# Kernel optimization log

Measured on AMD Instinct MI355X. Metric: run time of the kernel, lower is better.

Reference implementation:

```python
import jax, jax.numpy as jnp
import numpy as np
import math

N_HEADS = 16
EPS = 1e-6


def rmsnorm(x, w):
    xf = x.astype(jnp.float32)
    n = xf * jax.lax.rsqrt(jnp.mean(xf * xf, axis=-1, keepdims=True) + EPS)
    return n.astype(x.dtype) * w


def setup_inputs() -> dict:
    key = jax.random.key(0)
    ks = jax.random.split(key, 8)
    B, T, C, Hf = 1, 4096, 1024, 4096
    s = lambda fan_in: 1.0 / math.sqrt(fan_in)
    return {
        "x": jax.random.normal(ks[0], (B, T, C), jnp.float32),
        "attn_norm_w": jnp.ones((C,), jnp.float32),
        "ffn_norm_w": jnp.ones((C,), jnp.float32),
        "c_attn_w": jax.random.normal(ks[1], (3 * C, C), jnp.float32) * s(C),
        "c_proj_w": jax.random.normal(ks[2], (C, C), jnp.float32) * s(C),
        "w1": jax.random.normal(ks[3], (Hf, C), jnp.float32) * s(C),
        "w2": jax.random.normal(ks[4], (C, Hf), jnp.float32) * s(Hf),
        "w3": jax.random.normal(ks[5], (Hf, C), jnp.float32) * s(C),
    }


def attention(x, c_attn_w, c_proj_w):
    B, T, C = x.shape
    hd = C // N_HEADS
    qkv = x @ c_attn_w.T  # [B,T,3C]
    q, k, v = jnp.split(qkv, 3, axis=-1)
    q = q.reshape(B, T, N_HEADS, hd).transpose(0, 2, 1, 3)  # [B,H,T,hd]
    k = k.reshape(B, T, N_HEADS, hd).transpose(0, 2, 1, 3)
    v = v.reshape(B, T, N_HEADS, hd).transpose(0, 2, 1, 3)
    att = jnp.einsum('bhqd,bhkd->bhqk', q, k) * (1.0 / math.sqrt(hd))
    mask = jnp.tril(jnp.ones((T, T), bool))  # causal
    att = jnp.where(mask, att, -jnp.inf)
    att = jax.nn.softmax(att, axis=-1)
    y = jnp.einsum('bhqk,bhkd->bhqd', att, v)
    y = y.transpose(0, 2, 1, 3).reshape(B, T, C)
    return y @ c_proj_w.T


def ffn(x, w1, w2, w3):
    return (jax.nn.silu(x @ w1.T) * (x @ w3.T)) @ w2.T


def reference(x, attn_norm_w, ffn_norm_w, c_attn_w, c_proj_w, w1, w2, w3):
    x = x + attention(rmsnorm(x, attn_norm_w), c_attn_w, c_proj_w)
    x = x + ffn(rmsnorm(x, ffn_norm_w), w1, w2, w3)
    return x
```

## Files before the change

### kernel.cpp

```cpp
#include <hip/hip_runtime.h>
#include <hip/hip_bf16.h>

typedef __hip_bfloat16 bf16;
typedef __bf16 bf16r;
typedef bf16r bf16x8 __attribute__((ext_vector_type(8)));
typedef bf16r bf16x4 __attribute__((ext_vector_type(4)));
typedef float f32x4 __attribute__((ext_vector_type(4)));

#define T_SEQ 4096
#define C_DIM 1024
#define LD_QKV 3072
#define MB(x) ((size_t)(x) << 20)
#define SCL 0.18033688011112042f

#define AS1 __attribute__((address_space(1)))
#define AS3 __attribute__((address_space(3)))

static __device__ __forceinline__ unsigned short f2bf(float f) {
    bf16 h = (bf16)f;
    return *reinterpret_cast<unsigned short*>(&h);
}

__global__ __launch_bounds__(256) void cvt_w(const float* __restrict__ src, size_t eoff,
                                             ushort4* __restrict__ dst, int n4,
                                             int n4scl, float scl) {
    int i = blockIdx.x * 256 + threadIdx.x;
    const int stride = gridDim.x * 256;
    const float4* s = (const float4*)(src + eoff);
    for (; i < n4; i += stride) {
        float4 v = s[i];
        const float m = (i < n4scl) ? scl : 1.0f;
        ushort4 o;
        o.x = f2bf(v.x * m); o.y = f2bf(v.y * m); o.z = f2bf(v.z * m); o.w = f2bf(v.w * m);
        dst[i] = o;
    }
}

__global__ __launch_bounds__(256) void cvt_w13(const float* __restrict__ s1,
                                               const float* __restrict__ s3,
                                               ushort4* __restrict__ d1,
                                               ushort4* __restrict__ d3, int n4) {
    int i = blockIdx.x * 256 + threadIdx.x;
    const int stride = gridDim.x * 256;
    for (; i < n4; i += stride) {
        float4 v1 = ((const float4*)s1)[i];
        float4 v3 = ((const float4*)s3)[i];
        ushort4 o1, o3;
        o1.x = f2bf(v1.x); o1.y = f2bf(v1.y); o1.z = f2bf(v1.z); o1.w = f2bf(v1.w);
        o3.x = f2bf(v3.x); o3.y = f2bf(v3.y); o3.z = f2bf(v3.z); o3.w = f2bf(v3.w);
        d1[i] = o1;
        d3[i] = o3;
    }
}

__global__ __launch_bounds__(256) void copy_f32(const float4* __restrict__ src,
                                                float4* __restrict__ dst, int n4) {
    int i = blockIdx.x * 256 + threadIdx.x;
    const int stride = gridDim.x * 256;
    for (; i < n4; i += stride) dst[i] = src[i];
}

__global__ __launch_bounds__(256) void rmsnorm_k(const float* __restrict__ x,
                                                 const float* __restrict__ w,
                                                 bf16* __restrict__ out) {
    const int row = blockIdx.x;
    const int tid = threadIdx.x;
    const float* xr = x + (size_t)row * C_DIM;
    float v[4];
    float ss = 0.f;
#pragma unroll
    for (int i = 0; i < 4; i++) { v[i] = xr[tid * 4 + i]; ss += v[i] * v[i]; }
#pragma unroll
    for (int off = 32; off; off >>= 1) ss += __shfl_xor(ss, off);
    __shared__ float red[4];
    if ((tid & 63) == 0) red[tid >> 6] = ss;
    __syncthreads();
    const float tot = red[0] + red[1] + red[2] + red[3];
    const float scale = rsqrtf(tot * (1.0f / C_DIM) + 1e-6f);
#pragma unroll
    for (int i = 0; i < 4; i++) {
        const int c = tid * 4 + i;
        out[(size_t)row * C_DIM + c] = (bf16)(v[i] * scale * w[c]);
    }
}

template <int RESID, int OUTF32>
__global__ __launch_bounds__(256) void gemm128(const bf16* __restrict__ A, int lda,
                                               const bf16* __restrict__ B, int ldb,
                                               const void* __restrict__ resid,
                                               void* __restrict__ out,
                                               int N, int K) {
    __shared__ __align__(16) bf16r As[128 * 64];
    __shared__ __align__(16) bf16r Bs[128 * 64];
    const int tid = threadIdx.x;
    const int w = tid >> 6, lane = tid & 63;
    const int c = lane & 15, qd = lane >> 4;
    const int wm = w >> 1, wn = w & 1;
    const int mbase = blockIdx.y * 128;
    const int nbase = blockIdx.x * 128;
    const size_t koff = (size_t)blockIdx.z * K;

    const int srow = lane >> 3, schk = lane & 7;
    const bf16* gA = A + (size_t)(mbase + srow) * lda + schk * 8 + koff;
    const bf16* gB = B + (size_t)(nbase + srow) * ldb + schk * 8 + koff;

    f32x4 acc[4][4] = {};

    for (int k0 = 0; k0 < K; k0 += 64) {
        __syncthreads();
#pragma unroll
        for (int g = 0; g < 4; g++) {
            const int grp = w * 4 + g;
            __builtin_amdgcn_global_load_lds(
                (const AS1 void*)(gA + (size_t)(grp * 8) * lda + k0),
                (AS3 void*)&As[grp * 8 * 64], 16, 0, 0);
            __builtin_amdgcn_global_load_lds(
                (const AS1 void*)(gB + (size_t)(grp * 8) * ldb + k0),
                (AS3 void*)&Bs[grp * 8 * 64], 16, 0, 0);
        }
        __syncthreads();

#pragma unroll
        for (int kk = 0; kk < 2; kk++) {
            bf16x8 a[4], b[4];
#pragma unroll
            for (int i = 0; i < 4; i++)
                a[i] = *(const bf16x8*)&As[(wm * 64 + i * 16 + c) * 64 + kk * 32 + qd * 8];
#pragma unroll
            for (int j = 0; j < 4; j++)
                b[j] = *(const bf16x8*)&Bs[(wn * 64 + j * 16 + c) * 64 + kk * 32 + qd * 8];
#pragma unroll
            for (int i = 0; i < 4; i++)
#pragma unroll
                for (int j = 0; j < 4; j++)
                    acc[i][j] = __builtin_amdgcn_mfma_f32_16x16x32_bf16(a[i], b[j], acc[i][j], 0, 0, 0);
        }
    }

#pragma unroll
    for (int i = 0; i < 4; i++) {
#pragma unroll
        for (int j = 0; j < 4; j++) {
            const int col = nbase + wn * 64 + j * 16 + c;
#pragma unroll
            for (int reg = 0; reg < 4; reg++) {
                const int row = mbase + wm * 64 + i * 16 + qd * 4 + reg;
                const size_t idx = (size_t)row * N + col;
                float v = acc[i][j][reg];
                if (RESID == 2) v += ((const float*)resid)[idx];
                if (RESID == 3) {
                    const float a1 = (float)((const bf16*)resid)[idx];
                    v = (a1 / (1.0f + __expf(-a1))) * v;
                }
                if (RESID == 4) {
                    atomicAdd(&((float*)out)[idx], v);
                } else if (OUTF32) {
                    ((float*)out)[idx] = v;
                } else {
                    ((bf16*)out)[idx] = (bf16)v;
                }
            }
        }
    }
}

__global__ __launch_bounds__(256, 2) void gemm_w13(const bf16* __restrict__ A,
                                                   const bf16* __restrict__ B1,
                                                   const bf16* __restrict__ B3,
                                                   bf16* __restrict__ out,
                                                   int N, int K) {
    __shared__ __align__(16) bf16r As[128 * 64];
    __shared__ __align__(16) bf16r B1s[128 * 64];
    __shared__ __align__(16) bf16r B3s[128 * 64];
    const int tid = threadIdx.x;
    const int w = tid >> 6, lane = tid & 63;
    const int c = lane & 15, qd = lane >> 4;
    const int wm = w >> 1, wn = w & 1;
    const int mbase = blockIdx.y * 128;
    const int nbase = blockIdx.x * 128;

    const int srow = lane >> 3, schk = lane & 7;
    const bf16* gA = A + (size_t)(mbase + srow) * K + schk * 8;
    const bf16* gB1 = B1 + (size_t)(nbase + srow) * K + schk * 8;
    const bf16* gB3 = B3 + (size_t)(nbase + srow) * K + schk * 8;

    f32x4 acc1[4][4] = {};
    f32x4 acc3[4][4] = {};

    for (int k0 = 0; k0 < K; k0 += 64) {
        __syncthreads();
#pragma unroll
        for (int g = 0; g < 4; g++) {
            const int grp = w * 4 + g;
            __builtin_amdgcn_global_load_lds(
                (const AS1 void*)(gA + (size_t)(grp * 8) * K + k0),
                (AS3 void*)&As[grp * 8 * 64], 16, 0, 0);
            __builtin_amdgcn_global_load_lds(
                (const AS1 void*)(gB1 + (size_t)(grp * 8) * K + k0),
                (AS3 void*)&B1s[grp * 8 * 64], 16, 0, 0);
            __builtin_amdgcn_global_load_lds(
                (const AS1 void*)(gB3 + (size_t)(grp * 8) * K + k0),
                (AS3 void*)&B3s[grp * 8 * 64], 16, 0, 0);
        }
        __syncthreads();

#pragma unroll
        for (int kk = 0; kk < 2; kk++) {
            bf16x8 a[4], b1[4], b3[4];
#pragma unroll
            for (int i = 0; i < 4; i++)
                a[i] = *(const bf16x8*)&As[(wm * 64 + i * 16 + c) * 64 + kk * 32 + qd * 8];
#pragma unroll
            for (int j = 0; j < 4; j++) {
                b1[j] = *(const bf16x8*)&B1s[(wn * 64 + j * 16 + c) * 64 + kk * 32 + qd * 8];
                b3[j] = *(const bf16x8*)&B3s[(wn * 64 + j * 16 + c) * 64 + kk * 32 + qd * 8];
            }
#pragma unroll
            for (int i = 0; i < 4; i++)
#pragma unroll
                for (int j = 0; j < 4; j++) {
                    acc1[i][j] = __builtin_amdgcn_mfma_f32_16x16x32_bf16(a[i], b1[j], acc1[i][j], 0, 0, 0);
                    acc3[i][j] = __builtin_amdgcn_mfma_f32_16x16x32_bf16(a[i], b3[j], acc3[i][j], 0, 0, 0);
                }
        }
    }

#pragma unroll
    for (int i = 0; i < 4; i++) {
#pragma unroll
        for (int j = 0; j < 4; j++) {
            const int col = nbase + wn * 64 + j * 16 + c;
#pragma unroll
            for (int reg = 0; reg < 4; reg++) {
                const int row = mbase + wm * 64 + i * 16 + qd * 4 + reg;
                const float a1 = acc1[i][j][reg];
                const float h = (a1 / (1.0f + __expf(-a1))) * acc3[i][j][reg];
                out[(size_t)row * N + col] = (bf16)h;
            }
        }
    }
}

#define CTR_STRIDE 16
__global__ __launch_bounds__(256) void build_tr(const bf16* __restrict__ qkv,
                                                bf16* __restrict__ dst, int soff,
                                                int* __restrict__ ctrs) {
    if (blockIdx.x == 0 && blockIdx.y == 0 && threadIdx.x < 8 * CTR_STRIDE)
        ctrs[threadIdx.x] = 0;
    const int h = blockIdx.y;
    const int tb = blockIdx.x;
    __shared__ bf16 tile[64][65];
    const int tx = threadIdx.x & 63;
    const int ty = threadIdx.x >> 6;
    for (int rr = ty; rr < 64; rr += 4)
        tile[rr][tx] = qkv[(size_t)(tb * 64 + rr) * LD_QKV + soff + h * 64 + tx];
    __syncthreads();
    for (int rr = ty; rr < 64; rr += 4)
        dst[((size_t)h * 64 + rr) * T_SEQ + tb * 64 + tx] = tile[tx][rr];
}

__global__ __launch_bounds__(256) void attn_mfma(const bf16* __restrict__ qkv,
                                                 const bf16* __restrict__ VT,
                                                 bf16* __restrict__ y,
                                                 int* __restrict__ ctrs) {
    __shared__ __align__(16) bf16r Ks[128][64];
    __shared__ __align__(16) bf16r VTs[64][128];
    __shared__ __align__(16) bf16r Ps[4][16][128];
    __shared__ int s_wi;

    const int tid  = threadIdx.x;
    const int w    = tid >> 6;
    const int lane = tid & 63;
    const int c    = lane & 15;
    const int qd   = lane >> 4;
    const int sw   = c & 7;
    const int qi   = blockIdx.x & 7;
    int* ctr = ctrs + qi * CTR_STRIDE;

    while (true) {
        __syncthreads();
        if (tid == 0) s_wi = atomicAdd(ctr, 1);
        __syncthreads();
        const int j = s_wi;
        if (j >= 128) break;

        const int h    = qi + 8 * (j & 1);
        const int qb   = 63 - (j >> 1);
        const int qrow = qb * 64 + w * 16 + c;

        bf16x8 qf[2];
        {
            const bf16* qp = qkv + (size_t)qrow * LD_QKV + h * 64;
            qf[0] = *(const bf16x8*)(qp + qd * 8);
            qf[1] = *(const bf16x8*)(qp + 32 + qd * 8);
        }

        f32x4 O[4] = {};
        float m_i = -1e30f, l_i = 0.f;
        const int nkb = (qb >> 1) + 1;

        for (int kb = 0; kb < nkb; kb++) {
            __syncthreads();
#pragma unroll
            for (int ii = 0; ii < 4; ii++) {
                const int i = ii * 256 + tid;
                const int kr = i >> 3, ch = i & 7;
                *(bf16x8*)&Ks[kr][(ch ^ (kr & 7)) * 8] =
                    *(const bf16x8*)(qkv + (size_t)(kb * 128 + kr) * LD_QKV + C_DIM + h * 64 + ch * 8);
                const int vr = i >> 4, vch = i & 15;
                *(bf16x8*)&VTs[vr][(vch ^ (vr & 7)) * 8] =
                    *(const bf16x8*)(VT + ((size_t)h * 64 + vr) * T_SEQ + kb * 128 + vch * 8);
            }
            __syncthreads();

            f32x4 ST[8];
#pragma unroll
            for (int kt = 0; kt < 8; kt++) {
                f32x4 z = {};
#pragma unroll
                for (int ks = 0; ks < 2; ks++) {
                    bf16x8 kf = *(const bf16x8*)&Ks[kt * 16 + c][((ks * 4 + qd) ^ sw) * 8];
                    z = __builtin_amdgcn_mfma_f32_16x16x32_bf16(kf, qf[ks], z, 0, 0, 0);
                }
                ST[kt] = z;
            }

            if (kb == nkb - 1) {
#pragma unroll
                for (int kt = 0; kt < 8; kt++)
#pragma unroll
                    for (int r = 0; r < 4; r++)
                        if (kb * 128 + kt * 16 + qd * 4 + r > qrow) ST[kt][r] = -1e30f;
            }

            float mb = -1e30f;
#pragma unroll
            for (int kt = 0; kt < 8; kt++)
#pragma unroll
                for (int r = 0; r < 4; r++) mb = fmaxf(mb, ST[kt][r]);
            mb = fmaxf(mb, __shfl_xor(mb, 16));
            mb = fmaxf(mb, __shfl_xor(mb, 32));

            bf16x4 pv[8];
            float rs = 0.f;
            if (__all(mb - m_i <= 8.0f)) {
#pragma unroll
                for (int kt = 0; kt < 8; kt++)
#pragma unroll
                    for (int r = 0; r < 4; r++) {
                        const float p = exp2f(ST[kt][r] - m_i);
                        pv[kt][r] = (bf16r)p;
                        rs += p;
                    }
                rs += __shfl_xor(rs, 16);
                rs += __shfl_xor(rs, 32);
                l_i += rs;
            } else {
                const float mnew = fmaxf(m_i, mb);
                const float alpha = exp2f(m_i - mnew);
#pragma unroll
                for (int kt = 0; kt < 8; kt++)
#pragma unroll
                    for (int r = 0; r < 4; r++) {
                        const float p = exp2f(ST[kt][r] - mnew);
                        pv[kt][r] = (bf16r)p;
                        rs += p;
                    }
                rs += __shfl_xor(rs, 16);
                rs += __shfl_xor(rs, 32);
                l_i = l_i * alpha + rs;
                m_i = mnew;
#pragma unroll
                for (int dt = 0; dt < 4; dt++)
#pragma unroll
                    for (int r = 0; r < 4; r++) O[dt][r] *= alpha;
            }

#pragma unroll
            for (int kt = 0; kt < 8; kt++) {
                const int phys = (kt * 2 + (qd >> 1)) ^ sw;
                *(bf16x4*)&Ps[w][c][phys * 8 + (qd & 1) * 4] = pv[kt];
            }

#pragma unroll
            for (int ks = 0; ks < 4; ks++) {
                bf16x8 pf = *(const bf16x8*)&Ps[w][c][((ks * 4 + qd) ^ sw) * 8];
#pragma unroll
                for (int dt = 0; dt < 4; dt++) {
                    bf16x8 vf = *(const bf16x8*)&VTs[dt * 16 + c][((ks * 4 + qd) ^ sw) * 8];
                    O[dt] = __builtin_amdgcn_mfma_f32_16x16x32_bf16(vf, pf, O[dt], 0, 0, 0);
                }
            }
        }

        const float inv_l = 1.0f / l_i;
#pragma unroll
        for (int dt = 0; dt < 4; dt++) {
            bf16x4 ov;
#pragma unroll
            for (int r = 0; r < 4; r++) ov[r] = (bf16r)(O[dt][r] * inv_l);
            *(bf16x4*)(y + (size_t)qrow * C_DIM + h * 64 + dt * 16 + qd * 4) = ov;
        }
    }
}

extern "C" void kernel_launch(void* const* d_in, const int* in_sizes, int n_in,
                              void* d_out, int out_size, void* d_ws, size_t ws_size,
                              hipStream_t stream) {
    const float* x        = (const float*)d_in[0];
    const float* attn_w   = (const float*)d_in[1];
    const float* ffn_w    = (const float*)d_in[2];
    const float* c_attn_w = (const float*)d_in[3];
    const float* c_proj_w = (const float*)d_in[4];
    const float* w1       = (const float*)d_in[5];
    const float* w2       = (const float*)d_in[6];
    const float* w3       = (const float*)d_in[7];
    float* xmid = (float*)d_out;

    char* ws = (char*)d_ws;
    bf16* cwA  = (bf16*)(ws);
    bf16* cwP  = (bf16*)(ws + MB(6));
    bf16* rms1 = (bf16*)(ws + MB(8));
    bf16* qkv  = (bf16*)(ws + MB(16));
    bf16* VT   = (bf16*)(ws + MB(40));
    bf16* y    = (bf16*)(ws + MB(48));
    int*  ctrs = (int*)(ws + MB(8));
    bf16* rms2 = (bf16*)(ws);
    bf16* w1h  = (bf16*)(ws + MB(8));
    bf16* w3h  = (bf16*)(ws + MB(16));
    bf16* w2h  = (bf16*)(ws + MB(8));
    bf16* h1   = (bf16*)(ws + MB(24));

    cvt_w<<<512, 256, 0, stream>>>(c_attn_w, 0, (ushort4*)cwA, 3072 * 1024 / 4,
                                   1024 * 1024 / 4, SCL);
    cvt_w<<<512, 256, 0, stream>>>(c_proj_w, 0, (ushort4*)cwP, 1024 * 1024 / 4, 0, 1.0f);
    rmsnorm_k<<<T_SEQ, 256, 0, stream>>>(x, attn_w, rms1);
    gemm128<0, 0><<<dim3(24, 32), 256, 0, stream>>>(rms1, C_DIM, cwA, C_DIM, nullptr, qkv, 3072, 1024);
    build_tr<<<dim3(64, 16), 256, 0, stream>>>(qkv, VT, 2 * C_DIM, ctrs);
    attn_mfma<<<768, 256, 0, stream>>>(qkv, VT, y, ctrs);
    cvt_w13<<<512, 256, 0, stream>>>(w1, w3, (ushort4*)w1h, (ushort4*)w3h, 4096 * 1024 / 4);
    copy_f32<<<2048, 256, 0, stream>>>((const float4*)x, (float4*)xmid, T_SEQ * C_DIM / 4);
    gemm128<4, 1><<<dim3(8, 32, 2), 256, 0, stream>>>(y, C_DIM, cwP, C_DIM, nullptr, xmid, 1024, 512);
    rmsnorm_k<<<T_SEQ, 256, 0, stream>>>(xmid, ffn_w, rms2);
    gemm_w13<<<dim3(32, 32), 256, 0, stream>>>(rms2, w1h, w3h, h1, 4096, 1024);
    cvt_w<<<512, 256, 0, stream>>>(w2, 0, (ushort4*)w2h, 1024 * 4096 / 4, 0, 1.0f);
    gemm128<4, 1><<<dim3(8, 32, 4), 256, 0, stream>>>(h1, 4096, w2h, 4096, nullptr, xmid, 1024, 1024);
}
```

Before: 485.0 us.

## Split long causal attention rows into two KV halves with merge kernel

```diff
diff --git a/kernel.cpp b/kernel.cpp
--- a/kernel.cpp
+++ b/kernel.cpp
@@ -259,10 +259,35 @@
         dst[((size_t)h * 64 + rr) * T_SEQ + tb * 64 + tx] = tile[tx][rr];
 }
 
+struct SplitTab {
+    unsigned short v[192];
+    constexpr SplitTab() : v{} {
+        int idx = 0;
+        for (int s = 16; s >= 1; s--) {
+            for (int nkb = 17; nkb <= 32; nkb++)
+                if (nkb - (nkb >> 1) == s)
+                    for (int t = 1; t >= 0; t--)
+                        for (int hh = 0; hh < 2; hh++)
+                            v[idx++] = (unsigned short)(hh | (2 << 1) | ((2 * (nkb - 1) + t) << 3));
+            for (int nkb = 17; nkb <= 32; nkb++)
+                if ((nkb >> 1) == s)
+                    for (int t = 1; t >= 0; t--)
+                        for (int hh = 0; hh < 2; hh++)
+                            v[idx++] = (unsigned short)(hh | (1 << 1) | ((2 * (nkb - 1) + t) << 3));
+            for (int t = 1; t >= 0; t--)
+                for (int hh = 0; hh < 2; hh++)
+                    v[idx++] = (unsigned short)(hh | ((2 * (s - 1) + t) << 3));
+        }
+    }
+};
+static __device__ constexpr SplitTab g_tab{};
+
 __global__ __launch_bounds__(256) void attn_mfma(const bf16* __restrict__ qkv,
                                                  const bf16* __restrict__ VT,
                                                  bf16* __restrict__ y,
-                                                 int* __restrict__ ctrs) {
+                                                 int* __restrict__ ctrs,
+                                                 float* __restrict__ PO,
+                                                 float* __restrict__ ml) {
     __shared__ __align__(16) bf16r Ks[128][64];
     __shared__ __align__(16) bf16r VTs[64][128];
     __shared__ __align__(16) bf16r Ps[4][16][128];
@@ -282,11 +307,16 @@
         if (tid == 0) s_wi = atomicAdd(ctr, 1);
         __syncthreads();
         const int j = s_wi;
-        if (j >= 128) break;
-
-        const int h    = qi + 8 * (j & 1);
-        const int qb   = 63 - (j >> 1);
+        if (j >= 192) break;
+
+        const int e    = g_tab.v[j];
+        const int h    = qi + 8 * (e & 1);
+        const int part = (e >> 1) & 3;
+        const int qb   = e >> 3;
         const int qrow = qb * 64 + w * 16 + c;
+        const int nkb  = (qb >> 1) + 1;
+        const int kb0  = (part == 2) ? (nkb >> 1) : 0;
+        const int kb1  = (part == 1) ? (nkb >> 1) : nkb;
 
         bf16x8 qf[2];
         {
@@ -297,9 +327,8 @@
 
         f32x4 O[4] = {};
         float m_i = -1e30f, l_i = 0.f;
-        const int nkb = (qb >> 1) + 1;
-
-        for (int kb = 0; kb < nkb; kb++) {
+
+        for (int kb = kb0; kb < kb1; kb++) {
             __syncthreads();
 #pragma unroll
             for (int ii = 0; ii < 4; ii++) {
@@ -393,14 +422,54 @@
             }
         }
 
-        const float inv_l = 1.0f / l_i;
-#pragma unroll
-        for (int dt = 0; dt < 4; dt++) {
-            bf16x4 ov;
-#pragma unroll
-            for (int r = 0; r < 4; r++) ov[r] = (bf16r)(O[dt][r] * inv_l);
-            *(bf16x4*)(y + (size_t)qrow * C_DIM + h * 64 + dt * 16 + qd * 4) = ov;
-        }
+        if (part == 0) {
+            const float inv_l = 1.0f / l_i;
+#pragma unroll
+            for (int dt = 0; dt < 4; dt++) {
+                bf16x4 ov;
+#pragma unroll
+                for (int r = 0; r < 4; r++) ov[r] = (bf16r)(O[dt][r] * inv_l);
+                *(bf16x4*)(y + (size_t)qrow * C_DIM + h * 64 + dt * 16 + qd * 4) = ov;
+            }
+        } else {
+            const int ht = qb - 32;
+            const int ql = w * 16 + c;
+            const size_t pb = ((size_t)(h * 32 + ht) * 2 + (part - 1)) * 4096;
+#pragma unroll
+            for (int dt = 0; dt < 4; dt++)
+                *(f32x4*)&PO[pb + ql * 64 + dt * 16 + qd * 4] = O[dt];
+            if (qd == 0) {
+                const size_t mb_ = ((size_t)(h * 32 + ht) * 2 + (part - 1)) * 128;
+                ml[mb_ + ql * 2 + 0] = m_i;
+                ml[mb_ + ql * 2 + 1] = l_i;
+            }
+        }
+    }
+}
+
+__global__ __launch_bounds__(256) void attn_merge(const float* __restrict__ PO,
+                                                  const float* __restrict__ ml,
+                                                  bf16* __restrict__ y) {
+    const int ht = blockIdx.x, h = blockIdx.y;
+    const int tid = threadIdx.x;
+    const int q = tid >> 2;
+    const int d0 = (tid & 3) * 16;
+    const size_t pb = (size_t)(h * 32 + ht) * 2 * 4096;
+    const size_t mb_ = (size_t)(h * 32 + ht) * 2 * 128;
+    const float mA = ml[mb_ + q * 2 + 0],       lA = ml[mb_ + q * 2 + 1];
+    const float mB = ml[mb_ + 128 + q * 2 + 0], lB = ml[mb_ + 128 + q * 2 + 1];
+    const float m = fmaxf(mA, mB);
+    const float aA = exp2f(mA - m), aB = exp2f(mB - m);
+    const float inv = 1.0f / (lA * aA + lB * aB);
+    const size_t yb = (size_t)((ht + 32) * 64 + q) * C_DIM + h * 64 + d0;
+#pragma unroll
+    for (int dd = 0; dd < 16; dd += 4) {
+        f32x4 oa = *(const f32x4*)&PO[pb + q * 64 + d0 + dd];
+        f32x4 ob = *(const f32x4*)&PO[pb + 4096 + q * 64 + d0 + dd];
+        bf16x4 ov;
+#pragma unroll
+        for (int r = 0; r < 4; r++) ov[r] = (bf16r)((oa[r] * aA + ob[r] * aB) * inv);
+        *(bf16x4*)&y[yb + dd] = ov;
     }
 }
 
@@ -425,6 +494,8 @@
     bf16* VT   = (bf16*)(ws + MB(40));
     bf16* y    = (bf16*)(ws + MB(48));
     int*  ctrs = (int*)(ws + MB(8));
+    float* mlb = (float*)(ws);
+    float* POb = (float*)d_out;
     bf16* rms2 = (bf16*)(ws);
     bf16* w1h  = (bf16*)(ws + MB(8));
     bf16* w3h  = (bf16*)(ws + MB(16));
@@ -437,7 +508,8 @@
     rmsnorm_k<<<T_SEQ, 256, 0, stream>>>(x, attn_w, rms1);
     gemm128<0, 0><<<dim3(24, 32), 256, 0, stream>>>(rms1, C_DIM, cwA, C_DIM, nullptr, qkv, 3072, 1024);
     build_tr<<<dim3(64, 16), 256, 0, stream>>>(qkv, VT, 2 * C_DIM, ctrs);
-    attn_mfma<<<768, 256, 0, stream>>>(qkv, VT, y, ctrs);
+    attn_mfma<<<768, 256, 0, stream>>>(qkv, VT, y, ctrs, POb, mlb);
+    attn_merge<<<dim3(32, 16), 256, 0, stream>>>(POb, mlb, y);
     cvt_w13<<<512, 256, 0, stream>>>(w1, w3, (ushort4*)w1h, (ushort4*)w3h, 4096 * 1024 / 4);
     copy_f32<<<2048, 256, 0, stream>>>((const float4*)x, (float4*)xmid, T_SEQ * C_DIM / 4);
     gemm128<4, 1><<<dim3(8, 32, 2), 256, 0, stream>>>(y, C_DIM, cwP, C_DIM, nullptr, xmid, 1024, 512);
```

After: 536.9 us. 1.11x slower.
